# Optimization experiments

Hardware: AMD Instinct MI355X
Metric: run time of the kernel (lower is better)

Reference implementation:

```python
import jax, jax.numpy as jnp
import numpy as np

DIM = 512
HEADS = 16
DHEAD = DIM // HEADS
SQRT_DIM = float(np.sqrt(DIM))


def sinusoidal_pe(length, dim):
    # Transformer-XL style sinusoidal positional embedding, shape (length, dim)
    pos = jnp.arange(length, dtype=jnp.float32)[:, None]
    i = jnp.arange(0, dim, 2, dtype=jnp.float32)
    div = jnp.exp(-(jnp.log(jnp.float32(10000.0)) * i / dim))[None, :]
    ang = pos * div
    pe = jnp.zeros((length, dim), dtype=jnp.float32)
    pe = pe.at[:, 0::2].set(jnp.sin(ang)).at[:, 1::2].set(jnp.cos(ang))
    return pe


def rel_shift(x):
    # x: (B, H, L, M) -> Transformer-XL relative shift
    B, H, L, M = x.shape
    x = jnp.concatenate([jnp.zeros((B, H, L, 1), x.dtype), x], axis=-1)  # (B,H,L,M+1)
    x = x.reshape(B, H, M + 1, L)[:, :, 1:, :].reshape(B, H, L, M)
    return x


def setup_inputs() -> dict:
    key = jax.random.key(0)
    ks = jax.random.split(key, 16)
    B, L = 8, 1024
    s = 0.02
    return {
        "query": jax.random.normal(ks[0], (B, L, DIM), jnp.float32),
        "key_in": jax.random.normal(ks[1], (B, L, DIM), jnp.float32),
        "value": jax.random.normal(ks[2], (B, L, DIM), jnp.float32),
        "Wq": jax.random.normal(ks[3], (DIM, DIM), jnp.float32) * s,
        "bq": jnp.zeros((DIM,), jnp.float32),
        "Wk": jax.random.normal(ks[4], (DIM, DIM), jnp.float32) * s,
        "bk": jnp.zeros((DIM,), jnp.float32),
        "Wv": jax.random.normal(ks[5], (DIM, DIM), jnp.float32) * s,
        "bv": jnp.zeros((DIM,), jnp.float32),
        "Wpos": jax.random.normal(ks[6], (DIM, DIM), jnp.float32) * s,
        "u_bias": jax.random.normal(ks[7], (HEADS, DHEAD), jnp.float32) * s,
        "v_bias": jax.random.normal(ks[8], (HEADS, DHEAD), jnp.float32) * s,
        "Wo": jax.random.normal(ks[9], (DIM, DIM), jnp.float32) * s,
        "bo": jnp.zeros((DIM,), jnp.float32),
    }


def reference(query, key_in, value, Wq, bq, Wk, bk, Wv, bv, Wpos, u_bias, v_bias, Wo, bo):
    B, L, _ = value.shape
    pe = sinusoidal_pe(L, DIM)                                   # (L, dim)
    q = (query @ Wq.T + bq).reshape(B, L, HEADS, DHEAD)          # (B,L,H,d)
    k = (key_in @ Wk.T + bk).reshape(B, L, HEADS, DHEAD)         # (B,L,H,d)
    v = (value @ Wv.T + bv).reshape(B, L, HEADS, DHEAD)          # (B,L,H,d)
    pos = (pe @ Wpos.T).reshape(L, HEADS, DHEAD)                 # (L,H,d)

    content_score = jnp.einsum("blhd,bmhd->bhlm", q + u_bias, k)
    pos_score = jnp.einsum("blhd,mhd->bhlm", q + v_bias, pos)
    pos_score = rel_shift(pos_score)
    score = (content_score + pos_score) / SQRT_DIM               # (B,H,L,L)
    attn = jax.nn.softmax(score, axis=-1)
    context = jnp.einsum("bhlm,bmhd->blhd", attn, v).reshape(B, L, DIM)
    return context @ Wo.T + bo
```

## Files before the change

kernel.cpp:

```cpp
#include <hip/hip_runtime.h>
#include <hip/hip_bf16.h>
#include <cstddef>

typedef _Float16 f16;
typedef _Float16 f16x8 __attribute__((ext_vector_type(8)));
typedef _Float16 f16x4 __attribute__((ext_vector_type(4)));
typedef _Float16 f16x2 __attribute__((ext_vector_type(2)));
typedef float    f32x4 __attribute__((ext_vector_type(4)));

#define MFMA16(a,b,c) __builtin_amdgcn_mfma_f32_16x16x32_f16((a),(b),(c),0,0,0)

__device__ __forceinline__ void gload16(const void* g, void* lds) {
  __builtin_amdgcn_global_load_lds((const __attribute__((address_space(1))) void*)g,
                                   (__attribute__((address_space(3))) void*)lds, 16, 0, 0);
}

__global__ __launch_bounds__(256) void conv_w(
    const float* __restrict__ w0, const float* __restrict__ w1,
    const float* __restrict__ w2, const float* __restrict__ w3,
    const float* __restrict__ w4, f16* __restrict__ dst)
{
  const int idx = blockIdx.x * 256 + threadIdx.x;
  const int seg = idx >> 16;
  const int r   = idx & 65535;
  const float* s = seg == 0 ? w0 : seg == 1 ? w1 : seg == 2 ? w2 : seg == 3 ? w3 : w4;
  float4 v = ((const float4*)s)[r];
  f16x4 h = { (f16)v.x, (f16)v.y, (f16)v.z, (f16)v.w };
  ((f16x4*)(dst + ((size_t)seg << 18)))[r] = h;
}

__global__ __launch_bounds__(256) void pe16_kernel(f16* __restrict__ pe) {
  const int l = blockIdx.x;
  const int p = threadIdx.x;
  const float divv = expf(-(logf(10000.0f) * (2.0f * (float)p)) / 512.0f);
  const float ang  = (float)l * divv;
  f16x2 o = { (f16)sinf(ang), (f16)cosf(ang) };
  *(f16x2*)(pe + (size_t)l * 512 + 2 * p) = o;
}

template<int MODE, bool AF16>
__global__ __launch_bounds__(256) void gemm_k512(
    const void* __restrict__ Ap, const f16* __restrict__ Wf,
    const float* __restrict__ bias, void* __restrict__ Cp)
{
  __shared__ __align__(16) char Asm[8192];
  __shared__ __align__(16) char Bsm[8192];

  const int tid   = threadIdx.x;
  const int gm0   = blockIdx.x * 64;
  const int gn0   = blockIdx.y * 64;
  const int lane  = tid & 63, w = tid >> 6;
  const int row16 = lane & 15, grp = lane >> 4;
  const int wm = w & 1, wn = w >> 1;
  const int lr8  = lane >> 3;
  const int swcb = ((lane & 7) ^ lr8) * 16;

  f32x4 acc[2][2];
  for (int i = 0; i < 2; ++i) for (int j = 0; j < 2; ++j)
    for (int r = 0; r < 4; ++r) acc[i][j][r] = 0.f;

  for (int k0 = 0; k0 < 512; k0 += 64) {
    __syncthreads();
#pragma unroll
    for (int i = 0; i < 2; ++i) {
      const int rB = w * 8 + i * 32;
      gload16((const char*)Wf + ((size_t)(gn0 + rB + lr8)) * 1024 + (size_t)k0 * 2 + swcb,
              Bsm + rB * 128);
    }
    if constexpr (AF16) {
#pragma unroll
      for (int i = 0; i < 2; ++i) {
        const int rA = w * 8 + i * 32;
        gload16((const char*)Ap + ((size_t)(gm0 + rA + lr8)) * 1024 + (size_t)k0 * 2 + swcb,
                Asm + rA * 128);
      }
    } else {
#pragma unroll
      for (int i = 0; i < 4; ++i) {
        const int u = tid + i * 256;
        const int row = u >> 4, cf = (u & 15) * 4;
        float4 av = *(const float4*)((const float*)Ap + (size_t)(gm0 + row) * 512 + k0 + cf);
        f16x4 hv = { (f16)av.x, (f16)av.y, (f16)av.z, (f16)av.w };
        *(f16x4*)(Asm + row * 128 + ((cf * 2) ^ ((row & 7) * 16))) = hv;
      }
    }
    asm volatile("s_waitcnt vmcnt(0)" ::: "memory");
    __syncthreads();
#pragma unroll
    for (int kk = 0; kk < 64; kk += 32) {
      const int cb = (kk + 8 * grp) * 2;
      const int ra0 = wm * 32 + row16,      ra1 = ra0 + 16;
      const int rb0 = wn * 32 + row16,      rb1 = rb0 + 16;
      f16x8 a0 = *(const f16x8*)(Asm + ra0 * 128 + (cb ^ ((ra0 & 7) * 16)));
      f16x8 a1 = *(const f16x8*)(Asm + ra1 * 128 + (cb ^ ((ra1 & 7) * 16)));
      f16x8 b0 = *(const f16x8*)(Bsm + rb0 * 128 + (cb ^ ((rb0 & 7) * 16)));
      f16x8 b1 = *(const f16x8*)(Bsm + rb1 * 128 + (cb ^ ((rb1 & 7) * 16)));
      acc[0][0] = MFMA16(a0, b0, acc[0][0]);
      acc[0][1] = MFMA16(a0, b1, acc[0][1]);
      acc[1][0] = MFMA16(a1, b0, acc[1][0]);
      acc[1][1] = MFMA16(a1, b1, acc[1][1]);
    }
  }

  for (int fi = 0; fi < 2; ++fi) {
    for (int fj = 0; fj < 2; ++fj) {
      const int gc = gn0 + wn * 32 + fj * 16 + row16;
      float bval;
      if constexpr (MODE == 2) bval = 0.f; else bval = bias[gc];
      for (int r = 0; r < 4; ++r) {
        const int gr = gm0 + wm * 32 + fi * 16 + grp * 4 + r;
        const float v = acc[fi][fj][r] + bval;
        if constexpr (MODE == 0) {
          const int b = gr >> 10, l = gr & 1023, h = gc >> 5, d = gc & 31;
          ((f16*)Cp)[(((size_t)(b * 16 + h)) * 1024 + l) * 32 + d] = (f16)v;
        } else if constexpr (MODE == 1) {
          const int b = gr >> 10, l = gr & 1023, h = gc >> 5, d = gc & 31;
          ((f16*)Cp)[(((size_t)(b * 16 + h)) * 32 + d) * 1024 + l] = (f16)v;
        } else if constexpr (MODE == 2) {
          const int h = gc >> 5, d = gc & 31;
          ((f16*)Cp)[(((size_t)h) * 1024 + gr) * 32 + d] = (f16)v;
        } else {
          ((float*)Cp)[(size_t)gr * 512 + gc] = v;
        }
      }
    }
  }
}

__global__ __launch_bounds__(256) void attn_kernel(
    const f16* __restrict__ Qf, const f16* __restrict__ Kf,
    const f16* __restrict__ Vt, const f16* __restrict__ Pos,
    const float* __restrict__ ubias, const float* __restrict__ vbias,
    f16* __restrict__ ctx)
{
  __shared__ f16 P_lds[17][1028];
  __shared__ f16 ptile[4][16][72];

  const int tid   = threadIdx.x;
  const int w     = tid >> 6, lane = tid & 63;
  const int row16 = lane & 15, grp = lane >> 4;
  const int b = blockIdx.z, h = blockIdx.y;
  const int l0 = blockIdx.x * 16;

  const size_t bh = (size_t)(b * 16 + h);
  const f16* Qb = Qf + bh * 1024 * 32;
  const f16* Kb = Kf + bh * 1024 * 32;
  const f16* Vb = Vt + bh * 32 * 1024;
  const f16* Pb = Pos + (size_t)h * 1024 * 32;

  const f32x4 z4 = {0.f, 0.f, 0.f, 0.f};
  const float scale = 0.04419417382f;

  f16x8 qu, qv, qv2;
  {
    f16x8 qraw = *(const f16x8*)(Qb + (size_t)(l0 + row16) * 32 + 8 * grp);
    const int r2 = l0 + 16 + row16;
    f16x8 q2 = *(const f16x8*)(Qb + (size_t)(r2 < 1024 ? r2 : 1023) * 32 + 8 * grp);
#pragma unroll
    for (int e = 0; e < 8; ++e) {
      const float u = ubias[h * 32 + 8 * grp + e];
      const float v = vbias[h * 32 + 8 * grp + e];
      qu[e]  = (f16)((float)qraw[e] + u);
      qv[e]  = (f16)((float)qraw[e] + v);
      qv2[e] = (f16)((float)q2[e]   + v);
    }
  }

  if (tid < 17) {
    f16x4 z = {(f16)0.f, (f16)0.f, (f16)0.f, (f16)0.f};
    *(f16x4*)&P_lds[tid][1024] = z;
  }

#pragma unroll 4
  for (int c = 0; c < 16; ++c) {
    const int jc = w * 16 + c;
    f16x8 pf = *(const f16x8*)(Pb + (size_t)(jc * 16 + row16) * 32 + 8 * grp);
    f32x4 p0 = MFMA16(pf, qv,  z4);
    f32x4 p1 = MFMA16(pf, qv2, z4);
    const int j0 = jc * 16 + grp * 4;
    {
      f16x4 vv = { (f16)(p0[0] * scale), (f16)(p0[1] * scale),
                   (f16)(p0[2] * scale), (f16)(p0[3] * scale) };
      *(f16x4*)&P_lds[row16][j0] = vv;
    }
    if (row16 == 0) {
      f16x4 vv = { (f16)(p1[0] * scale), (f16)(p1[1] * scale),
                   (f16)(p1[2] * scale), (f16)(p1[3] * scale) };
      *(f16x4*)&P_lds[16][j0] = vv;
    }
  }
  __syncthreads();

  float psum = 0.f;
  f32x4 od[2];
#pragma unroll
  for (int hh = 0; hh < 2; ++hh) for (int r = 0; r < 4; ++r) od[hh][r] = 0.f;

  const int  c1 = 1023 - l0 - row16;
  const int  rowoff = row16 * 1028;
  const f16* Pbase = &P_lds[0][0];

  for (int ti = 0; ti < 4; ++ti) {
    const int mbase = w * 256 + ti * 64;
    f32x4 st[4];
#pragma unroll
    for (int c = 0; c < 4; ++c) {
      f16x8 kf = *(const f16x8*)(Kb + (size_t)(mbase + c * 16 + row16) * 32 + 8 * grp);
      st[c] = MFMA16(kf, qu, z4);
    }
#pragma unroll
    for (int c = 0; c < 4; ++c) {
      float p[4];
#pragma unroll
      for (int r = 0; r < 4; ++r) {
        const int jA  = mbase + c * 16 + grp * 4 + r + c1;
        const int idx = rowoff + jA + (jA >= 1025 ? 3 : 0);
        const float sh = (float)Pbase[idx];
        const float s  = fmaf(st[c][r], scale, sh);
        p[r] = __expf(s);
        psum += p[r];
      }
      f16x4 pv = { (f16)p[0], (f16)p[1], (f16)p[2], (f16)p[3] };
      *(f16x4*)&ptile[w][row16][c * 16 + grp * 4] = pv;
    }
#pragma unroll
    for (int kc = 0; kc < 2; ++kc) {
      f16x8 pa = *(const f16x8*)&ptile[w][row16][kc * 32 + 8 * grp];
#pragma unroll
      for (int hh = 0; hh < 2; ++hh) {
        f16x8 vf = *(const f16x8*)(Vb + (size_t)(hh * 16 + row16) * 1024 + mbase + kc * 32 + 8 * grp);
        od[hh] = MFMA16(pa, vf, od[hh]);
      }
    }
  }

  float l1 = psum + __shfl_xor(psum, 16);
  l1 += __shfl_xor(l1, 32);

  __syncthreads();
  float* mo = (float*)&P_lds[0][0];
  float* ls = mo + 4 * 16 * 32;
#pragma unroll
  for (int hh = 0; hh < 2; ++hh)
#pragma unroll
    for (int r = 0; r < 4; ++r)
      mo[(w * 16 + grp * 4 + r) * 32 + hh * 16 + row16] = od[hh][r];
  if (grp == 0) ls[w * 16 + row16] = l1;
  __syncthreads();

  const int q = tid >> 4, dp = tid & 15;
  const float Ls = ls[q] + ls[16 + q] + ls[32 + q] + ls[48 + q];
  float o0 = 0.f, o1 = 0.f;
#pragma unroll
  for (int ww = 0; ww < 4; ++ww) {
    o0 += mo[(ww * 16 + q) * 32 + 2 * dp];
    o1 += mo[(ww * 16 + q) * 32 + 2 * dp + 1];
  }
  const float inv = 1.f / Ls;
  const size_t oidx = ((size_t)(b * 1024 + l0 + q)) * 512 + h * 32 + 2 * dp;
  f16x2 o2 = { (f16)(o0 * inv), (f16)(o1 * inv) };
  *(f16x2*)(ctx + oidx) = o2;
}

extern "C" void kernel_launch(void* const* d_in, const int* in_sizes, int n_in,
                              void* d_out, int out_size, void* d_ws, size_t ws_size,
                              hipStream_t stream) {
  const float* query  = (const float*)d_in[0];
  const float* key_in = (const float*)d_in[1];
  const float* value  = (const float*)d_in[2];
  const float* Wq = (const float*)d_in[3];
  const float* bq = (const float*)d_in[4];
  const float* Wk = (const float*)d_in[5];
  const float* bk = (const float*)d_in[6];
  const float* Wv = (const float*)d_in[7];
  const float* bv = (const float*)d_in[8];
  const float* Wpos = (const float*)d_in[9];
  const float* ub   = (const float*)d_in[10];
  const float* vb   = (const float*)d_in[11];
  const float* Wo = (const float*)d_in[12];
  const float* bo = (const float*)d_in[13];
  float* out = (float*)d_out;

  char* ws = (char*)d_ws;
  f16* W16  = (f16*)(ws);
  f16* pe16 = (f16*)(ws + 2621440);
  f16* Qf   = (f16*)(ws + 3670016);
  f16* Kf   = (f16*)(ws + 12058624);
  f16* Vtf  = (f16*)(ws + 20447232);
  f16* Pf   = (f16*)(ws + 28835840);
  f16* ctx  = (f16*)(ws + 29884416);

  conv_w<<<1280, 256, 0, stream>>>(Wq, Wk, Wv, Wpos, Wo, W16);
  pe16_kernel<<<1024, 256, 0, stream>>>(pe16);
  gemm_k512<0, false><<<dim3(128, 8), 256, 0, stream>>>(query,  W16,          bq, Qf);
  gemm_k512<0, false><<<dim3(128, 8), 256, 0, stream>>>(key_in, W16 + 262144, bk, Kf);
  gemm_k512<1, false><<<dim3(128, 8), 256, 0, stream>>>(value,  W16 + 524288, bv, Vtf);
  gemm_k512<2, true ><<<dim3(16,  8), 256, 0, stream>>>(pe16,   W16 + 786432, nullptr, Pf);
  attn_kernel<<<dim3(64, 16, 8), 256, 0, stream>>>(Qf, Kf, Vtf, Pf, ub, vb, ctx);
  gemm_k512<3, true ><<<dim3(128, 8), 256, 0, stream>>>(ctx, W16 + 1048576, bo, out);
}
```

Measured before the change: 303.7 us.

## Feed softmax probs straight to K16 MFMA, use exp2, fast-path shift reads

```diff
diff --git a/kernel.cpp b/kernel.cpp
--- a/kernel.cpp
+++ b/kernel.cpp
@@ -8,7 +8,14 @@
 typedef _Float16 f16x2 __attribute__((ext_vector_type(2)));
 typedef float    f32x4 __attribute__((ext_vector_type(4)));
 
-#define MFMA16(a,b,c) __builtin_amdgcn_mfma_f32_16x16x32_f16((a),(b),(c),0,0,0)
+#define MFMA16(a,b,c)   __builtin_amdgcn_mfma_f32_16x16x32_f16((a),(b),(c),0,0,0)
+#define MFMA16K16(a,b,c) __builtin_amdgcn_mfma_f32_16x16x16f16((a),(b),(c),0,0,0)
+
+#if __has_builtin(__builtin_amdgcn_exp2f)
+#define EXP2(x) __builtin_amdgcn_exp2f(x)
+#else
+#define EXP2(x) __expf((x) * 0.6931471805599453f)
+#endif
 
 __device__ __forceinline__ void gload16(const void* g, void* lds) {
   __builtin_amdgcn_global_load_lds((const __attribute__((address_space(1))) void*)g,
@@ -134,7 +141,6 @@
     f16* __restrict__ ctx)
 {
   __shared__ f16 P_lds[17][1028];
-  __shared__ f16 ptile[4][16][72];
 
   const int tid   = threadIdx.x;
   const int w     = tid >> 6, lane = tid & 63;
@@ -149,7 +155,7 @@
   const f16* Pb = Pos + (size_t)h * 1024 * 32;
 
   const f32x4 z4 = {0.f, 0.f, 0.f, 0.f};
-  const float scale = 0.04419417382f;
+  const float kpre = 0.0637587157f;
 
   f16x8 qu, qv, qv2;
   {
@@ -179,13 +185,13 @@
     f32x4 p1 = MFMA16(pf, qv2, z4);
     const int j0 = jc * 16 + grp * 4;
     {
-      f16x4 vv = { (f16)(p0[0] * scale), (f16)(p0[1] * scale),
-                   (f16)(p0[2] * scale), (f16)(p0[3] * scale) };
+      f16x4 vv = { (f16)(p0[0] * kpre), (f16)(p0[1] * kpre),
+                   (f16)(p0[2] * kpre), (f16)(p0[3] * kpre) };
       *(f16x4*)&P_lds[row16][j0] = vv;
     }
     if (row16 == 0) {
-      f16x4 vv = { (f16)(p1[0] * scale), (f16)(p1[1] * scale),
-                   (f16)(p1[2] * scale), (f16)(p1[3] * scale) };
+      f16x4 vv = { (f16)(p1[0] * kpre), (f16)(p1[1] * kpre),
+                   (f16)(p1[2] * kpre), (f16)(p1[3] * kpre) };
       *(f16x4*)&P_lds[16][j0] = vv;
     }
   }
@@ -196,41 +202,54 @@
 #pragma unroll
   for (int hh = 0; hh < 2; ++hh) for (int r = 0; r < 4; ++r) od[hh][r] = 0.f;
 
-  const int  c1 = 1023 - l0 - row16;
-  const int  rowoff = row16 * 1028;
-  const f16* Pbase = &P_lds[0][0];
+  const int  c1   = 1023 - l0 - row16;
+  const f16* Prow = &P_lds[row16][0];
+  const f16* Vr0  = Vb + (size_t)row16 * 1024;
+  const f16* Vr1  = Vb + (size_t)(16 + row16) * 1024;
 
   for (int ti = 0; ti < 4; ++ti) {
     const int mbase = w * 256 + ti * 64;
+
     f32x4 st[4];
 #pragma unroll
     for (int c = 0; c < 4; ++c) {
       f16x8 kf = *(const f16x8*)(Kb + (size_t)(mbase + c * 16 + row16) * 32 + 8 * grp);
       st[c] = MFMA16(kf, qu, z4);
     }
+
+    float sh[4][4];
+    const bool unifB = (mbase >= l0 + 17);
+    const bool unifA = (mbase + 62 <= l0);
+    if (unifB | unifA) {
+      const f16* pp = Prow + mbase + grp * 4 + c1 + (unifB ? 3 : 0);
+#pragma unroll
+      for (int c = 0; c < 4; ++c)
+#pragma unroll
+        for (int r = 0; r < 4; ++r) sh[c][r] = (float)pp[c * 16 + r];
+    } else {
+#pragma unroll
+      for (int c = 0; c < 4; ++c)
+#pragma unroll
+        for (int r = 0; r < 4; ++r) {
+          const int jA = mbase + c * 16 + grp * 4 + r + c1;
+          sh[c][r] = (float)Prow[jA + (jA >= 1025 ? 3 : 0)];
+        }
+    }
+
 #pragma unroll
     for (int c = 0; c < 4; ++c) {
       float p[4];
 #pragma unroll
       for (int r = 0; r < 4; ++r) {
-        const int jA  = mbase + c * 16 + grp * 4 + r + c1;
-        const int idx = rowoff + jA + (jA >= 1025 ? 3 : 0);
-        const float sh = (float)Pbase[idx];
-        const float s  = fmaf(st[c][r], scale, sh);
-        p[r] = __expf(s);
+        p[r] = EXP2(fmaf(st[c][r], kpre, sh[c][r]));
         psum += p[r];
       }
-      f16x4 pv = { (f16)p[0], (f16)p[1], (f16)p[2], (f16)p[3] };
-      *(f16x4*)&ptile[w][row16][c * 16 + grp * 4] = pv;
-    }
-#pragma unroll
-    for (int kc = 0; kc < 2; ++kc) {
-      f16x8 pa = *(const f16x8*)&ptile[w][row16][kc * 32 + 8 * grp];
-#pragma unroll
-      for (int hh = 0; hh < 2; ++hh) {
-        f16x8 vf = *(const f16x8*)(Vb + (size_t)(hh * 16 + row16) * 1024 + mbase + kc * 32 + 8 * grp);
-        od[hh] = MFMA16(pa, vf, od[hh]);
-      }
+      f16x4 pa = { (f16)p[0], (f16)p[1], (f16)p[2], (f16)p[3] };
+      const int m0 = mbase + c * 16 + grp * 4;
+      f16x4 v0 = *(const f16x4*)(Vr0 + m0);
+      f16x4 v1 = *(const f16x4*)(Vr1 + m0);
+      od[0] = MFMA16K16(pa, v0, od[0]);
+      od[1] = MFMA16K16(pa, v1, od[1]);
     }
   }
 
```

Measured after the change: 345.7 us. 13.8% more time.

## Enlarge GEMM tiles to 128x128 and merge Q/K/V projections into one launch

Applied to the files above, without the earlier changes.

```diff
diff --git a/kernel.cpp b/kernel.cpp
--- a/kernel.cpp
+++ b/kernel.cpp
@@ -38,85 +38,170 @@
   *(f16x2*)(pe + (size_t)l * 512 + 2 * p) = o;
 }
 
-template<int MODE, bool AF16>
-__global__ __launch_bounds__(256) void gemm_k512(
-    const void* __restrict__ Ap, const f16* __restrict__ Wf,
-    const float* __restrict__ bias, void* __restrict__ Cp)
+__global__ __launch_bounds__(256) void gemm128_qkv(
+    const float* __restrict__ q_in, const float* __restrict__ k_in,
+    const float* __restrict__ v_in, const f16* __restrict__ W16,
+    const float* __restrict__ bq, const float* __restrict__ bk,
+    const float* __restrict__ bv,
+    f16* __restrict__ Qf, f16* __restrict__ Kf, f16* __restrict__ Vtf)
 {
-  __shared__ __align__(16) char Asm[8192];
-  __shared__ __align__(16) char Bsm[8192];
+  __shared__ __align__(16) char Asm[16384];
+  __shared__ __align__(16) char Bsm[16384];
+
+  const int z = blockIdx.z;
+  const float* Ap   = z == 0 ? q_in : z == 1 ? k_in : v_in;
+  const f16*   Wf   = W16 + (size_t)z * 262144;
+  const float* bias = z == 0 ? bq : z == 1 ? bk : bv;
+  f16*         Cp   = z == 0 ? Qf : z == 1 ? Kf : Vtf;
 
   const int tid   = threadIdx.x;
-  const int gm0   = blockIdx.x * 64;
-  const int gn0   = blockIdx.y * 64;
+  const int gm0   = blockIdx.x * 128;
+  const int gn0   = blockIdx.y * 128;
   const int lane  = tid & 63, w = tid >> 6;
   const int row16 = lane & 15, grp = lane >> 4;
   const int wm = w & 1, wn = w >> 1;
   const int lr8  = lane >> 3;
   const int swcb = ((lane & 7) ^ lr8) * 16;
 
-  f32x4 acc[2][2];
-  for (int i = 0; i < 2; ++i) for (int j = 0; j < 2; ++j)
-    for (int r = 0; r < 4; ++r) acc[i][j][r] = 0.f;
+  f32x4 acc[4][4];
+#pragma unroll
+  for (int i = 0; i < 4; ++i)
+#pragma unroll
+    for (int j = 0; j < 4; ++j)
+#pragma unroll
+      for (int r = 0; r < 4; ++r) acc[i][j][r] = 0.f;
 
   for (int k0 = 0; k0 < 512; k0 += 64) {
     __syncthreads();
-#pragma unroll
-    for (int i = 0; i < 2; ++i) {
-      const int rB = w * 8 + i * 32;
+    float4 areg[8];
+#pragma unroll
+    for (int i = 0; i < 8; ++i) {
+      const int u = tid + i * 256;
+      const int row = u >> 4, cf = (u & 15) * 4;
+      areg[i] = *(const float4*)(Ap + (size_t)(gm0 + row) * 512 + k0 + cf);
+    }
+#pragma unroll
+    for (int i = 0; i < 4; ++i) {
+      const int rB = w * 32 + i * 8;
       gload16((const char*)Wf + ((size_t)(gn0 + rB + lr8)) * 1024 + (size_t)k0 * 2 + swcb,
               Bsm + rB * 128);
     }
-    if constexpr (AF16) {
-#pragma unroll
-      for (int i = 0; i < 2; ++i) {
-        const int rA = w * 8 + i * 32;
-        gload16((const char*)Ap + ((size_t)(gm0 + rA + lr8)) * 1024 + (size_t)k0 * 2 + swcb,
-                Asm + rA * 128);
-      }
-    } else {
-#pragma unroll
-      for (int i = 0; i < 4; ++i) {
-        const int u = tid + i * 256;
-        const int row = u >> 4, cf = (u & 15) * 4;
-        float4 av = *(const float4*)((const float*)Ap + (size_t)(gm0 + row) * 512 + k0 + cf);
-        f16x4 hv = { (f16)av.x, (f16)av.y, (f16)av.z, (f16)av.w };
-        *(f16x4*)(Asm + row * 128 + ((cf * 2) ^ ((row & 7) * 16))) = hv;
-      }
+#pragma unroll
+    for (int i = 0; i < 8; ++i) {
+      const int u = tid + i * 256;
+      const int row = u >> 4, cf = (u & 15) * 4;
+      f16x4 hv = { (f16)areg[i].x, (f16)areg[i].y, (f16)areg[i].z, (f16)areg[i].w };
+      *(f16x4*)(Asm + row * 128 + ((cf * 2) ^ ((row & 7) * 16))) = hv;
     }
     asm volatile("s_waitcnt vmcnt(0)" ::: "memory");
     __syncthreads();
 #pragma unroll
     for (int kk = 0; kk < 64; kk += 32) {
       const int cb = (kk + 8 * grp) * 2;
-      const int ra0 = wm * 32 + row16,      ra1 = ra0 + 16;
-      const int rb0 = wn * 32 + row16,      rb1 = rb0 + 16;
-      f16x8 a0 = *(const f16x8*)(Asm + ra0 * 128 + (cb ^ ((ra0 & 7) * 16)));
-      f16x8 a1 = *(const f16x8*)(Asm + ra1 * 128 + (cb ^ ((ra1 & 7) * 16)));
-      f16x8 b0 = *(const f16x8*)(Bsm + rb0 * 128 + (cb ^ ((rb0 & 7) * 16)));
-      f16x8 b1 = *(const f16x8*)(Bsm + rb1 * 128 + (cb ^ ((rb1 & 7) * 16)));
-      acc[0][0] = MFMA16(a0, b0, acc[0][0]);
-      acc[0][1] = MFMA16(a0, b1, acc[0][1]);
-      acc[1][0] = MFMA16(a1, b0, acc[1][0]);
-      acc[1][1] = MFMA16(a1, b1, acc[1][1]);
-    }
-  }
-
-  for (int fi = 0; fi < 2; ++fi) {
-    for (int fj = 0; fj < 2; ++fj) {
-      const int gc = gn0 + wn * 32 + fj * 16 + row16;
+      f16x8 af[4], bf[4];
+#pragma unroll
+      for (int f = 0; f < 4; ++f) {
+        const int ra = wm * 64 + f * 16 + row16;
+        const int rb = wn * 64 + f * 16 + row16;
+        af[f] = *(const f16x8*)(Asm + ra * 128 + (cb ^ ((ra & 7) * 16)));
+        bf[f] = *(const f16x8*)(Bsm + rb * 128 + (cb ^ ((rb & 7) * 16)));
+      }
+#pragma unroll
+      for (int fi = 0; fi < 4; ++fi)
+#pragma unroll
+        for (int fj = 0; fj < 4; ++fj)
+          acc[fi][fj] = MFMA16(af[fi], bf[fj], acc[fi][fj]);
+    }
+  }
+
+#pragma unroll
+  for (int fi = 0; fi < 4; ++fi)
+#pragma unroll
+    for (int fj = 0; fj < 4; ++fj) {
+      const int gc = gn0 + wn * 64 + fj * 16 + row16;
+      const float bval = bias[gc];
+#pragma unroll
+      for (int r = 0; r < 4; ++r) {
+        const int gr = gm0 + wm * 64 + fi * 16 + grp * 4 + r;
+        const float v = acc[fi][fj][r] + bval;
+        const int b = gr >> 10, l = gr & 1023, h = gc >> 5, d = gc & 31;
+        if (z != 2) {
+          Cp[(((size_t)(b * 16 + h)) * 1024 + l) * 32 + d] = (f16)v;
+        } else {
+          Cp[(((size_t)(b * 16 + h)) * 32 + d) * 1024 + l] = (f16)v;
+        }
+      }
+    }
+}
+
+template<int MODE>
+__global__ __launch_bounds__(256) void gemm128_f16(
+    const f16* __restrict__ Ap, const f16* __restrict__ Wf,
+    const float* __restrict__ bias, void* __restrict__ Cp)
+{
+  __shared__ __align__(16) char Asm[16384];
+  __shared__ __align__(16) char Bsm[16384];
+
+  const int tid   = threadIdx.x;
+  const int gm0   = blockIdx.x * 128;
+  const int gn0   = blockIdx.y * 128;
+  const int lane  = tid & 63, w = tid >> 6;
+  const int row16 = lane & 15, grp = lane >> 4;
+  const int wm = w & 1, wn = w >> 1;
+  const int lr8  = lane >> 3;
+  const int swcb = ((lane & 7) ^ lr8) * 16;
+
+  f32x4 acc[4][4];
+#pragma unroll
+  for (int i = 0; i < 4; ++i)
+#pragma unroll
+    for (int j = 0; j < 4; ++j)
+#pragma unroll
+      for (int r = 0; r < 4; ++r) acc[i][j][r] = 0.f;
+
+  for (int k0 = 0; k0 < 512; k0 += 64) {
+    __syncthreads();
+#pragma unroll
+    for (int i = 0; i < 4; ++i) {
+      const int rr = w * 32 + i * 8;
+      gload16((const char*)Ap + ((size_t)(gm0 + rr + lr8)) * 1024 + (size_t)k0 * 2 + swcb,
+              Asm + rr * 128);
+      gload16((const char*)Wf + ((size_t)(gn0 + rr + lr8)) * 1024 + (size_t)k0 * 2 + swcb,
+              Bsm + rr * 128);
+    }
+    asm volatile("s_waitcnt vmcnt(0)" ::: "memory");
+    __syncthreads();
+#pragma unroll
+    for (int kk = 0; kk < 64; kk += 32) {
+      const int cb = (kk + 8 * grp) * 2;
+      f16x8 af[4], bf[4];
+#pragma unroll
+      for (int f = 0; f < 4; ++f) {
+        const int ra = wm * 64 + f * 16 + row16;
+        const int rb = wn * 64 + f * 16 + row16;
+        af[f] = *(const f16x8*)(Asm + ra * 128 + (cb ^ ((ra & 7) * 16)));
+        bf[f] = *(const f16x8*)(Bsm + rb * 128 + (cb ^ ((rb & 7) * 16)));
+      }
+#pragma unroll
+      for (int fi = 0; fi < 4; ++fi)
+#pragma unroll
+        for (int fj = 0; fj < 4; ++fj)
+          acc[fi][fj] = MFMA16(af[fi], bf[fj], acc[fi][fj]);
+    }
+  }
+
+#pragma unroll
+  for (int fi = 0; fi < 4; ++fi)
+#pragma unroll
+    for (int fj = 0; fj < 4; ++fj) {
+      const int gc = gn0 + wn * 64 + fj * 16 + row16;
       float bval;
       if constexpr (MODE == 2) bval = 0.f; else bval = bias[gc];
+#pragma unroll
       for (int r = 0; r < 4; ++r) {
-        const int gr = gm0 + wm * 32 + fi * 16 + grp * 4 + r;
+        const int gr = gm0 + wm * 64 + fi * 16 + grp * 4 + r;
         const float v = acc[fi][fj][r] + bval;
-        if constexpr (MODE == 0) {
-          const int b = gr >> 10, l = gr & 1023, h = gc >> 5, d = gc & 31;
-          ((f16*)Cp)[(((size_t)(b * 16 + h)) * 1024 + l) * 32 + d] = (f16)v;
-        } else if constexpr (MODE == 1) {
-          const int b = gr >> 10, l = gr & 1023, h = gc >> 5, d = gc & 31;
-          ((f16*)Cp)[(((size_t)(b * 16 + h)) * 32 + d) * 1024 + l] = (f16)v;
-        } else if constexpr (MODE == 2) {
+        if constexpr (MODE == 2) {
           const int h = gc >> 5, d = gc & 31;
           ((f16*)Cp)[(((size_t)h) * 1024 + gr) * 32 + d] = (f16)v;
         } else {
@@ -124,7 +209,6 @@
         }
       }
     }
-  }
 }
 
 __global__ __launch_bounds__(256) void attn_kernel(
@@ -196,9 +280,8 @@
 #pragma unroll
   for (int hh = 0; hh < 2; ++hh) for (int r = 0; r < 4; ++r) od[hh][r] = 0.f;
 
-  const int  c1 = 1023 - l0 - row16;
-  const int  rowoff = row16 * 1028;
-  const f16* Pbase = &P_lds[0][0];
+  const int  c1   = 1023 - l0 - row16;
+  const f16* Prow = &P_lds[row16][0];
 
   for (int ti = 0; ti < 4; ++ti) {
     const int mbase = w * 256 + ti * 64;
@@ -214,8 +297,8 @@
 #pragma unroll
       for (int r = 0; r < 4; ++r) {
         const int jA  = mbase + c * 16 + grp * 4 + r + c1;
-        const int idx = rowoff + jA + (jA >= 1025 ? 3 : 0);
-        const float sh = (float)Pbase[idx];
+        const int idx = jA + (jA >= 1025 ? 3 : 0);
+        const float sh = (float)Prow[idx];
         const float s  = fmaf(st[c][r], scale, sh);
         p[r] = __expf(s);
         psum += p[r];
@@ -292,10 +375,9 @@
 
   conv_w<<<1280, 256, 0, stream>>>(Wq, Wk, Wv, Wpos, Wo, W16);
   pe16_kernel<<<1024, 256, 0, stream>>>(pe16);
-  gemm_k512<0, false><<<dim3(128, 8), 256, 0, stream>>>(query,  W16,          bq, Qf);
-  gemm_k512<0, false><<<dim3(128, 8), 256, 0, stream>>>(key_in, W16 + 262144, bk, Kf);
-  gemm_k512<1, false><<<dim3(128, 8), 256, 0, stream>>>(value,  W16 + 524288, bv, Vtf);
-  gemm_k512<2, true ><<<dim3(16,  8), 256, 0, stream>>>(pe16,   W16 + 786432, nullptr, Pf);
+  gemm128_qkv<<<dim3(64, 4, 3), 256, 0, stream>>>(query, key_in, value, W16,
+                                                  bq, bk, bv, Qf, Kf, Vtf);
+  gemm128_f16<2><<<dim3(8,  4), 256, 0, stream>>>(pe16, W16 + 786432, nullptr, Pf);
   attn_kernel<<<dim3(64, 16, 8), 256, 0, stream>>>(Qf, Kf, Vtf, Pf, ub, vb, ctx);
-  gemm_k512<3, true ><<<dim3(128, 8), 256, 0, stream>>>(ctx, W16 + 1048576, bo, out);
-}
+  gemm128_f16<3><<<dim3(64, 4), 256, 0, stream>>>(ctx, W16 + 1048576, bo, out);
+}
```

New measurement: 319.5 us. 5.2% more time.
